# Performance work log

Measured on AMD Instinct MI355X. Metric: run time of the kernel, lower is better.

The kernel has to match this reference:

```python
import jax, jax.numpy as jnp
import numpy as np

L, B, E, H = 2048, 2, 1024, 16
HD = E // H


def setup_inputs() -> dict:
    key = jax.random.key(0)
    ks = jax.random.split(key, 7)
    return {
        "query": jax.random.normal(ks[0], (L, B, E), dtype=jnp.float32),
        "key": jax.random.normal(ks[1], (L, B, E), dtype=jnp.float32),
        "value": jax.random.normal(ks[2], (L, B, E), dtype=jnp.float32),
        "in_proj_weight": jax.random.normal(ks[3], (3 * E, E), dtype=jnp.float32) * 0.02,
        "in_proj_bias": jax.random.normal(ks[4], (3 * E,), dtype=jnp.float32) * 0.02,
        "out_proj_weight": jax.random.normal(ks[5], (E, E), dtype=jnp.float32) * 0.02,
        "out_proj_bias": jax.random.normal(ks[6], (E,), dtype=jnp.float32) * 0.02,
    }


def reference(query, key, value, in_proj_weight, in_proj_bias, out_proj_weight, out_proj_bias):
    l, b, e = query.shape
    scaling = jnp.asarray(HD, query.dtype) ** -0.5
    wq, wk, wv = jnp.split(in_proj_weight, 3, axis=0)
    bq, bk, bv = jnp.split(in_proj_bias, 3)
    q = (query @ wq.T + bq) * scaling          # [L,B,E]
    k = key @ wk.T + bk
    v = value @ wv.T + bv

    def to_heads(t):  # [L,B,E] -> [B*H, L, HD]
        return t.reshape(l, b * H, HD).transpose(1, 0, 2)

    q, k, v = to_heads(q), to_heads(k), to_heads(v)
    scores = jnp.einsum('nld,nmd->nlm', q, k)  # [B*H, L, L] materialized as in legacy MHA
    attn = jax.nn.softmax(scores, axis=-1)
    out = jnp.einsum('nlm,nmd->nld', attn, v)  # [B*H, L, HD]
    out = out.transpose(1, 0, 2).reshape(l, b, e)
    return out @ out_proj_weight.T + out_proj_bias
```

## Files before the change

### kernel.cpp

```cpp
#include <hip/hip_runtime.h>
#include <hip/hip_bf16.h>

typedef __attribute__((ext_vector_type(8))) short short8;
typedef __attribute__((ext_vector_type(4))) float floatx4;
typedef __attribute__((ext_vector_type(16))) float floatx16;

#define L_SEQ 2048
#define EMB   1024
#define HD    64
#define QSCALE 0.18033688011112042f
#define FIXMAX2 11.541560327111707f

__device__ __forceinline__ unsigned short f2bf(float f) {
    unsigned int u = __float_as_uint(f);
    u += 0x7fffu + ((u >> 16) & 1u);
    return (unsigned short)(u >> 16);
}
__device__ __forceinline__ unsigned pkbf(float a, float b) {
    return (unsigned)f2bf(a) | ((unsigned)f2bf(b) << 16);
}
__device__ __forceinline__ unsigned pkbf2(float a, float b) {
    __hip_bfloat162 h = __float22bfloat162_rn(make_float2(a, b));
    unsigned u; __builtin_memcpy(&u, &h, 4); return u;
}
__device__ __forceinline__ void gld_lds16(const void* g, void* l) {
    __builtin_amdgcn_global_load_lds(
        (const __attribute__((address_space(1))) unsigned*)g,
        (__attribute__((address_space(3))) unsigned*)l, 16, 0, 0);
}
__device__ __forceinline__ float fexp2(float x) {
    return __builtin_amdgcn_exp2f(x);
}

__global__ __launch_bounds__(256) void convert_all(
    const float* __restrict__ q, const float* __restrict__ k,
    const float* __restrict__ v, const float* __restrict__ ipw,
    const float* __restrict__ opw,
    unsigned short* __restrict__ Abq, unsigned short* __restrict__ Abk,
    unsigned short* __restrict__ Abv, unsigned short* __restrict__ Wipb,
    unsigned short* __restrict__ Wopb)
{
    const int NA = 1048576, NIP = 786432;
    int idx = blockIdx.x * 256 + threadIdx.x;
    const float* src; unsigned short* dst; int o;
    if (idx < NA)            { src = q;   dst = Abq;  o = idx; }
    else if (idx < 2 * NA)   { src = k;   dst = Abk;  o = idx - NA; }
    else if (idx < 3 * NA)   { src = v;   dst = Abv;  o = idx - 2 * NA; }
    else if (idx < 3 * NA + NIP) { src = ipw; dst = Wipb; o = idx - 3 * NA; }
    else                     { src = opw; dst = Wopb; o = idx - 3 * NA - NIP; }
    float4 f = ((const float4*)src)[o];
    ((uint2*)dst)[o] = make_uint2(pkbf(f.x, f.y), pkbf(f.z, f.w));
}

__global__ __launch_bounds__(256, 3) void qkv_gemm(
    const unsigned short* __restrict__ Abq, const unsigned short* __restrict__ Abk,
    const unsigned short* __restrict__ Abv, const unsigned short* __restrict__ Wb,
    const float* __restrict__ Bip,
    unsigned short* __restrict__ Qh, unsigned short* __restrict__ Kf,
    unsigned short* __restrict__ Vf)
{
    __shared__ unsigned short lds[17408];
    unsigned short* As = lds;
    unsigned short* Bs = lds + 8192;

    const int tid = threadIdx.x, lane = tid & 63, w = tid >> 6;
    const int wm = (w & 1) * 64, wn = (w >> 1) * 64;
    const int m0 = blockIdx.x * 128, n0 = blockIdx.y * 128;
    const int cn = lane & 15, g = lane >> 4;
    const int z = n0 >> 10;
    const unsigned short* Ag = (z == 0) ? Abq : (z == 1) ? Abk : Abv;

    floatx4 acc[4][4];
    #pragma unroll
    for (int i = 0; i < 4; ++i)
        #pragma unroll
        for (int j = 0; j < 4; ++j) acc[i][j] = (floatx4){0.f, 0.f, 0.f, 0.f};

    for (int k0 = 0; k0 < EMB; k0 += 64) {
        __syncthreads();
        #pragma unroll
        for (int p = 0; p < 4; ++p) {
            int u0 = (p * 4 + w) * 64, u = u0 + lane, row = u >> 3, sl = u & 7;
            gld_lds16(Ag + (size_t)(m0 + row) * EMB + k0 + ((sl ^ (row & 7)) * 8), &As[u0 * 8]);
            gld_lds16(Wb + (size_t)(n0 + row) * EMB + k0 + ((sl ^ (row & 7)) * 8), &Bs[u0 * 8]);
        }
        __syncthreads();
        #pragma unroll
        for (int kc = 0; kc < 2; ++kc) {
            short8 a4[4], b4[4];
            #pragma unroll
            for (int i = 0; i < 4; ++i)
                a4[i] = *(const short8*)&As[(wm + i * 16 + cn) * 64 + (((kc * 4 + g) ^ (cn & 7)) * 8)];
            #pragma unroll
            for (int j = 0; j < 4; ++j)
                b4[j] = *(const short8*)&Bs[(wn + j * 16 + cn) * 64 + (((kc * 4 + g) ^ (cn & 7)) * 8)];
            #pragma unroll
            for (int i = 0; i < 4; ++i)
                #pragma unroll
                for (int j = 0; j < 4; ++j)
                    acc[i][j] = __builtin_amdgcn_mfma_f32_16x16x32_bf16(a4[i], b4[j], acc[i][j], 0, 0, 0);
        }
    }

    if (z == 0) {
        #pragma unroll
        for (int j = 0; j < 4; ++j) {
            int col = n0 + wn + j * 16 + cn;
            float bv = Bip[col];
            int o = col & 1023, h = o >> 6, d = o & 63;
            #pragma unroll
            for (int i = 0; i < 4; ++i)
                #pragma unroll
                for (int r = 0; r < 4; ++r) {
                    int rr = m0 + wm + i * 16 + g * 4 + r;
                    float vv = acc[i][j][r] + bv;
                    int l = rr >> 1, bb = rr & 1, nn = bb * 16 + h;
                    Qh[((size_t)nn * L_SEQ + l) * HD + d] = f2bf(vv * QSCALE);
                }
        }
    } else if (z == 1) {
        __syncthreads();
        #pragma unroll
        for (int j = 0; j < 4; ++j) {
            int cl = wn + j * 16 + cn;
            float bv = Bip[n0 + cl];
            #pragma unroll
            for (int i = 0; i < 4; ++i)
                #pragma unroll
                for (int r = 0; r < 4; ++r) {
                    int rr = wm + i * 16 + g * 4 + r;
                    lds[rr * 136 + cl] = f2bf(acc[i][j][r] + bv);
                }
        }
        __syncthreads();
        const int h0 = (n0 - 1024) >> 6;
        const int b = w >> 1, hl = w & 1;
        const int nn = b * 16 + h0 + hl;
        const int c32l = lane & 31, hi5 = lane >> 5;
        #pragma unroll
        for (int cc = 0; cc < 8; ++cc) {
            int t32l = cc >> 2, kk = cc & 3;
            int rr = (t32l * 32 + c32l) * 2 + b;
            int ccol = hl * 64 + kk * 16 + hi5 * 8;
            uint4 val = *(const uint4*)&lds[rr * 136 + ccol];
            int ck = (nn * 64 + (m0 >> 6) + t32l) * 4 + kk;
            *(uint4*)(Kf + (size_t)ck * 512 + lane * 8) = val;
        }
    } else {
        __syncthreads();
        #pragma unroll
        for (int j = 0; j < 4; ++j) {
            int col_l = wn + j * 16 + cn;
            float bv = Bip[n0 + col_l];
            #pragma unroll
            for (int i = 0; i < 4; ++i) {
                int rrb = wm + i * 16 + g * 4;
                int l0 = rrb >> 1;
                float v0 = acc[i][j][0] + bv, v1 = acc[i][j][1] + bv;
                float v2 = acc[i][j][2] + bv, v3 = acc[i][j][3] + bv;
                *(unsigned*)&lds[col_l * 136 +      l0] = pkbf(v0, v2);
                *(unsigned*)&lds[col_l * 136 + 64 + l0] = pkbf(v1, v3);
            }
        }
        __syncthreads();
        const int h0 = (n0 - 2048) >> 6;
        const int b = w >> 1, hl = w & 1;
        const int nn = b * 16 + h0 + hl;
        const int c32l = lane & 31, hi5 = lane >> 5;
        #pragma unroll
        for (int cc = 0; cc < 8; ++cc) {
            int dt = cc >> 2, kk2l = cc & 3;
            int col_l = hl * 64 + dt * 32 + c32l;
            int keyl = kk2l * 16 + hi5 * 8;
            uint4 val = *(const uint4*)&lds[col_l * 136 + b * 64 + keyl];
            int cv = nn * 256 + ((m0 >> 5) + kk2l) * 2 + dt;
            *(uint4*)(Vf + (size_t)cv * 512 + lane * 8) = val;
        }
    }
}

__global__ __launch_bounds__(256, 2) void flash_attn_k(
    const unsigned short* __restrict__ Qh, const unsigned short* __restrict__ Kf,
    const unsigned short* __restrict__ Vf, unsigned short* __restrict__ Oh)
{
    const int id = blockIdx.y * 32 + blockIdx.x;
    const int xcd = id & 7, slot = id >> 3;
    const int n = xcd * 4 + (slot & 3);
    const int q0 = (slot >> 2) * 64;

    __shared__ float Uf[2 * 64 * 67];

    const int tid = threadIdx.x, lane = tid & 63, w = tid >> 6;
    const int c32 = lane & 31, hi = lane >> 5;

    short8 qf[2][4];
    #pragma unroll
    for (int qt = 0; qt < 2; ++qt)
        #pragma unroll
        for (int kk = 0; kk < 4; ++kk)
            qf[qt][kk] = *(const short8*)(Qh + ((size_t)n * L_SEQ + q0 + qt * 32 + c32) * HD + kk * 16 + hi * 8);

    floatx16 acc_o[2][2];
    #pragma unroll
    for (int qt = 0; qt < 2; ++qt)
        #pragma unroll
        for (int dt = 0; dt < 2; ++dt)
            #pragma unroll
            for (int r = 0; r < 16; ++r) acc_o[qt][dt][r] = 0.f;
    float lsum0 = 0.f, lsum1 = 0.f;

    const unsigned short* kp = Kf + ((size_t)n * 256 + w * 64) * 512 + lane * 8;
    const unsigned short* vp = Vf + ((size_t)n * 256 + w * 64) * 512 + lane * 8;

    for (int t = 0; t < 16; ++t) {
        short8 kf[4], vf[2][2];
        #pragma unroll
        for (int kk = 0; kk < 4; ++kk)
            kf[kk] = *(const short8*)(kp + kk * 512);
        #pragma unroll
        for (int kc = 0; kc < 2; ++kc)
            #pragma unroll
            for (int dt = 0; dt < 2; ++dt)
                vf[kc][dt] = *(const short8*)(vp + (kc * 2 + dt) * 512);
        kp += 2048; vp += 2048;

        floatx16 s[2];
        #pragma unroll
        for (int qt = 0; qt < 2; ++qt) {
            #pragma unroll
            for (int r = 0; r < 16; ++r) s[qt][r] = -FIXMAX2;
            __builtin_amdgcn_s_setprio(1);
            #pragma unroll
            for (int kk = 0; kk < 4; ++kk)
                s[qt] = __builtin_amdgcn_mfma_f32_32x32x16_bf16(kf[kk], qf[qt][kk], s[qt], 0, 0, 0);
            __builtin_amdgcn_s_setprio(0);
        }

        #pragma unroll
        for (int qt = 0; qt < 2; ++qt) {
            float p[16];
            #pragma unroll
            for (int r = 0; r < 16; ++r) p[r] = fexp2(s[qt][r]);
            float ls = ((p[0] + p[1]) + (p[2] + p[3])) + ((p[4] + p[5]) + (p[6] + p[7]))
                     + ((p[8] + p[9]) + (p[10] + p[11])) + ((p[12] + p[13]) + (p[14] + p[15]));
            if (qt == 0) lsum0 += ls; else lsum1 += ls;

            short8 pa[2];
            #pragma unroll
            for (int kc = 0; kc < 2; ++kc) {
                unsigned A = pkbf2(p[kc * 8 + 0], p[kc * 8 + 1]);
                unsigned B = pkbf2(p[kc * 8 + 2], p[kc * 8 + 3]);
                unsigned C = pkbf2(p[kc * 8 + 4], p[kc * 8 + 5]);
                unsigned D = pkbf2(p[kc * 8 + 6], p[kc * 8 + 7]);
                asm("v_permlane32_swap_b32 %0, %1" : "+v"(A), "+v"(C));
                asm("v_permlane32_swap_b32 %0, %1" : "+v"(B), "+v"(D));
                union { unsigned u[4]; short8 v; } cv;
                cv.u[0] = A; cv.u[1] = B; cv.u[2] = C; cv.u[3] = D;
                pa[kc] = cv.v;
            }

            __builtin_amdgcn_s_setprio(1);
            #pragma unroll
            for (int kc = 0; kc < 2; ++kc)
                #pragma unroll
                for (int dt = 0; dt < 2; ++dt)
                    acc_o[qt][dt] = __builtin_amdgcn_mfma_f32_32x32x16_bf16(pa[kc], vf[kc][dt], acc_o[qt][dt], 0, 0, 0);
            __builtin_amdgcn_s_setprio(0);
        }
    }

    {
        float a0 = lsum0, b0 = lsum0;
        asm("v_permlane32_swap_b32 %0, %1" : "+v"(a0), "+v"(b0));
        lsum0 = a0 + b0;
        float a1 = lsum1, b1 = lsum1;
        asm("v_permlane32_swap_b32 %0, %1" : "+v"(a1), "+v"(b1));
        lsum1 = a1 + b1;
    }

#define BLOB_STORE(base) do {                                              \
    _Pragma("unroll")                                                      \
    for (int qt = 0; qt < 2; ++qt)                                         \
        _Pragma("unroll")                                                  \
        for (int dt = 0; dt < 2; ++dt)                                     \
            _Pragma("unroll")                                              \
            for (int r = 0; r < 16; ++r)                                   \
                Uf[(base) + (qt * 2 + dt) * 16 + r] = acc_o[qt][dt][r];    \
    Uf[(base) + 64] = lsum0; Uf[(base) + 65] = lsum1;                      \
} while (0)
#define BLOB_ADD(base) do {                                                \
    _Pragma("unroll")                                                      \
    for (int qt = 0; qt < 2; ++qt)                                         \
        _Pragma("unroll")                                                  \
        for (int dt = 0; dt < 2; ++dt)                                     \
            _Pragma("unroll")                                              \
            for (int r = 0; r < 16; ++r)                                   \
                acc_o[qt][dt][r] += Uf[(base) + (qt * 2 + dt) * 16 + r];   \
    lsum0 += Uf[(base) + 64]; lsum1 += Uf[(base) + 65];                    \
} while (0)

    const int r0 = lane * 67, r1 = 64 * 67 + lane * 67;
    __syncthreads();
    if (w == 1) BLOB_STORE(r0);
    if (w == 3) BLOB_STORE(r1);
    __syncthreads();
    if (w == 0) BLOB_ADD(r0);
    if (w == 2) { BLOB_ADD(r1); BLOB_STORE(r1); }
    __syncthreads();
    if (w == 0) {
        BLOB_ADD(r1);
        float inv0 = 1.0f / lsum0, inv1 = 1.0f / lsum1;
        const int hib = hi * 16;
        const int bb = n >> 4, h = n & 15;
        #pragma unroll
        for (int qt = 0; qt < 2; ++qt) {
            float invq = qt ? inv1 : inv0;
            #pragma unroll
            for (int r = 0; r < 16; ++r) {
                int idx = ((r & 3) + 8 * (r >> 2)) * 4 + hib;
                float invr = __int_as_float(__builtin_amdgcn_ds_bpermute(idx, __float_as_int(invq)));
                int q = q0 + qt * 32 + (r & 3) + 8 * (r >> 2) + hi * 4;
                #pragma unroll
                for (int dt = 0; dt < 2; ++dt) {
                    int e = h * 64 + dt * 32 + c32;
                    Oh[((size_t)q * 2 + bb) * EMB + e] = f2bf(acc_o[qt][dt][r] * invr);
                }
            }
        }
    }
#undef BLOB_STORE
#undef BLOB_ADD
}

__global__ __launch_bounds__(256, 3) void out_gemm(
    const unsigned short* __restrict__ Oh, const unsigned short* __restrict__ Wob,
    const float* __restrict__ bo, float* __restrict__ out)
{
    __shared__ unsigned short As[128 * 64];
    __shared__ unsigned short Bs[128 * 64];

    const int tid = threadIdx.x, lane = tid & 63, w = tid >> 6;
    const int wm = (w & 1) * 64, wn = (w >> 1) * 64;
    const int m0 = blockIdx.x * 128, n0 = blockIdx.y * 128;
    const int cn = lane & 15, g = lane >> 4;

    floatx4 acc[4][4];
    #pragma unroll
    for (int i = 0; i < 4; ++i)
        #pragma unroll
        for (int j = 0; j < 4; ++j) acc[i][j] = (floatx4){0.f, 0.f, 0.f, 0.f};

    for (int k0 = 0; k0 < EMB; k0 += 64) {
        __syncthreads();
        #pragma unroll
        for (int p = 0; p < 4; ++p) {
            int u0 = (p * 4 + w) * 64, u = u0 + lane, row = u >> 3, sl = u & 7;
            gld_lds16(Oh  + (size_t)(m0 + row) * EMB + k0 + ((sl ^ (row & 7)) * 8), &As[u0 * 8]);
            gld_lds16(Wob + (size_t)(n0 + row) * EMB + k0 + ((sl ^ (row & 7)) * 8), &Bs[u0 * 8]);
        }
        __syncthreads();
        #pragma unroll
        for (int kc = 0; kc < 2; ++kc) {
            short8 a4[4], b4[4];
            #pragma unroll
            for (int i = 0; i < 4; ++i)
                a4[i] = *(const short8*)&As[(wm + i * 16 + cn) * 64 + (((kc * 4 + g) ^ (cn & 7)) * 8)];
            #pragma unroll
            for (int j = 0; j < 4; ++j)
                b4[j] = *(const short8*)&Bs[(wn + j * 16 + cn) * 64 + (((kc * 4 + g) ^ (cn & 7)) * 8)];
            #pragma unroll
            for (int i = 0; i < 4; ++i)
                #pragma unroll
                for (int j = 0; j < 4; ++j)
                    acc[i][j] = __builtin_amdgcn_mfma_f32_16x16x32_bf16(a4[i], b4[j], acc[i][j], 0, 0, 0);
        }
    }

    #pragma unroll
    for (int j = 0; j < 4; ++j) {
        int col = n0 + wn + j * 16 + cn;
        float bv = bo[col];
        #pragma unroll
        for (int i = 0; i < 4; ++i)
            #pragma unroll
            for (int r = 0; r < 4; ++r)
                out[(size_t)(m0 + wm + i * 16 + g * 4 + r) * EMB + col] = acc[i][j][r] + bv;
    }
}

extern "C" void kernel_launch(void* const* d_in, const int* in_sizes, int n_in,
                              void* d_out, int out_size, void* d_ws, size_t ws_size,
                              hipStream_t stream) {
    const float* q   = (const float*)d_in[0];
    const float* k   = (const float*)d_in[1];
    const float* v   = (const float*)d_in[2];
    const float* ipw = (const float*)d_in[3];
    const float* ipb = (const float*)d_in[4];
    const float* opw = (const float*)d_in[5];
    const float* opb = (const float*)d_in[6];
    float* out = (float*)d_out;

    const size_t HE = (size_t)32 * L_SEQ * HD;
    unsigned short* Qh   = (unsigned short*)d_ws;
    unsigned short* Kf   = Qh + HE;
    unsigned short* Vf   = Kf + HE;
    unsigned short* Wipb = Vf + HE;
    unsigned short* Wopb = Wipb + (size_t)3 * EMB * EMB;
    unsigned short* Abq  = Wopb + (size_t)EMB * EMB;
    unsigned short* Abk  = Abq + HE;
    unsigned short* Abv  = Abk + HE;
    unsigned short* Oh   = Abq;

    convert_all<<<dim3(16384), 256, 0, stream>>>(q, k, v, ipw, opw, Abq, Abk, Abv, Wipb, Wopb);
    qkv_gemm<<<dim3(32, 24), 256, 0, stream>>>(Abq, Abk, Abv, Wipb, ipb, Qh, Kf, Vf);
    flash_attn_k<<<dim3(32, 32), 256, 0, stream>>>(Qh, Kf, Vf, Oh);
    out_gemm<<<dim3(32, 8), 256, 0, stream>>>(Oh, Wopb, opb, out);
}
```

Baseline: 210.7 us.

## Stage Q epilogue through LDS into fragment layout; halve out_gemm M tile

```diff
diff --git a/kernel.cpp b/kernel.cpp
--- a/kernel.cpp
+++ b/kernel.cpp
@@ -56,7 +56,7 @@
     const unsigned short* __restrict__ Abq, const unsigned short* __restrict__ Abk,
     const unsigned short* __restrict__ Abv, const unsigned short* __restrict__ Wb,
     const float* __restrict__ Bip,
-    unsigned short* __restrict__ Qh, unsigned short* __restrict__ Kf,
+    unsigned short* __restrict__ Qf, unsigned short* __restrict__ Kf,
     unsigned short* __restrict__ Vf)
 {
     __shared__ unsigned short lds[17408];
@@ -102,23 +102,10 @@
         }
     }
 
-    if (z == 0) {
-        #pragma unroll
-        for (int j = 0; j < 4; ++j) {
-            int col = n0 + wn + j * 16 + cn;
-            float bv = Bip[col];
-            int o = col & 1023, h = o >> 6, d = o & 63;
-            #pragma unroll
-            for (int i = 0; i < 4; ++i)
-                #pragma unroll
-                for (int r = 0; r < 4; ++r) {
-                    int rr = m0 + wm + i * 16 + g * 4 + r;
-                    float vv = acc[i][j][r] + bv;
-                    int l = rr >> 1, bb = rr & 1, nn = bb * 16 + h;
-                    Qh[((size_t)nn * L_SEQ + l) * HD + d] = f2bf(vv * QSCALE);
-                }
-        }
-    } else if (z == 1) {
+    const int c32l = lane & 31, hi5 = lane >> 5;
+    const int b = w >> 1, hl = w & 1;
+
+    if (z < 2) {
         __syncthreads();
         #pragma unroll
         for (int j = 0; j < 4; ++j) {
@@ -129,14 +116,14 @@
                 #pragma unroll
                 for (int r = 0; r < 4; ++r) {
                     int rr = wm + i * 16 + g * 4 + r;
-                    lds[rr * 136 + cl] = f2bf(acc[i][j][r] + bv);
+                    float vv = acc[i][j][r] + bv;
+                    lds[rr * 136 + cl] = f2bf(z == 0 ? vv * QSCALE : vv);
                 }
         }
         __syncthreads();
-        const int h0 = (n0 - 1024) >> 6;
-        const int b = w >> 1, hl = w & 1;
+        const int h0 = (n0 & 1023) >> 6;
         const int nn = b * 16 + h0 + hl;
-        const int c32l = lane & 31, hi5 = lane >> 5;
+        unsigned short* Dst = (z == 0) ? Qf : Kf;
         #pragma unroll
         for (int cc = 0; cc < 8; ++cc) {
             int t32l = cc >> 2, kk = cc & 3;
@@ -144,7 +131,7 @@
             int ccol = hl * 64 + kk * 16 + hi5 * 8;
             uint4 val = *(const uint4*)&lds[rr * 136 + ccol];
             int ck = (nn * 64 + (m0 >> 6) + t32l) * 4 + kk;
-            *(uint4*)(Kf + (size_t)ck * 512 + lane * 8) = val;
+            *(uint4*)(Dst + (size_t)ck * 512 + lane * 8) = val;
         }
     } else {
         __syncthreads();
@@ -164,9 +151,7 @@
         }
         __syncthreads();
         const int h0 = (n0 - 2048) >> 6;
-        const int b = w >> 1, hl = w & 1;
         const int nn = b * 16 + h0 + hl;
-        const int c32l = lane & 31, hi5 = lane >> 5;
         #pragma unroll
         for (int cc = 0; cc < 8; ++cc) {
             int dt = cc >> 2, kk2l = cc & 3;
@@ -180,7 +165,7 @@
 }
 
 __global__ __launch_bounds__(256, 2) void flash_attn_k(
-    const unsigned short* __restrict__ Qh, const unsigned short* __restrict__ Kf,
+    const unsigned short* __restrict__ Qf, const unsigned short* __restrict__ Kf,
     const unsigned short* __restrict__ Vf, unsigned short* __restrict__ Oh)
 {
     const int id = blockIdx.y * 32 + blockIdx.x;
@@ -198,7 +183,7 @@
     for (int qt = 0; qt < 2; ++qt)
         #pragma unroll
         for (int kk = 0; kk < 4; ++kk)
-            qf[qt][kk] = *(const short8*)(Qh + ((size_t)n * L_SEQ + q0 + qt * 32 + c32) * HD + kk * 16 + hi * 8);
+            qf[qt][kk] = *(const short8*)(Qf + ((size_t)((n * 64 + (q0 >> 5) + qt) * 4 + kk)) * 512 + lane * 8);
 
     floatx16 acc_o[2][2];
     #pragma unroll
@@ -332,21 +317,21 @@
 #undef BLOB_ADD
 }
 
-__global__ __launch_bounds__(256, 3) void out_gemm(
+__global__ __launch_bounds__(256, 4) void out_gemm(
     const unsigned short* __restrict__ Oh, const unsigned short* __restrict__ Wob,
     const float* __restrict__ bo, float* __restrict__ out)
 {
-    __shared__ unsigned short As[128 * 64];
+    __shared__ unsigned short As[64 * 64];
     __shared__ unsigned short Bs[128 * 64];
 
     const int tid = threadIdx.x, lane = tid & 63, w = tid >> 6;
-    const int wm = (w & 1) * 64, wn = (w >> 1) * 64;
-    const int m0 = blockIdx.x * 128, n0 = blockIdx.y * 128;
+    const int wm = (w & 1) * 32, wn = (w >> 1) * 64;
+    const int m0 = blockIdx.x * 64, n0 = blockIdx.y * 128;
     const int cn = lane & 15, g = lane >> 4;
 
-    floatx4 acc[4][4];
+    floatx4 acc[2][4];
     #pragma unroll
-    for (int i = 0; i < 4; ++i)
+    for (int i = 0; i < 2; ++i)
         #pragma unroll
         for (int j = 0; j < 4; ++j) acc[i][j] = (floatx4){0.f, 0.f, 0.f, 0.f};
 
@@ -355,21 +340,22 @@
         #pragma unroll
         for (int p = 0; p < 4; ++p) {
             int u0 = (p * 4 + w) * 64, u = u0 + lane, row = u >> 3, sl = u & 7;
-            gld_lds16(Oh  + (size_t)(m0 + row) * EMB + k0 + ((sl ^ (row & 7)) * 8), &As[u0 * 8]);
+            if (p < 2)
+                gld_lds16(Oh + (size_t)(m0 + row) * EMB + k0 + ((sl ^ (row & 7)) * 8), &As[u0 * 8]);
             gld_lds16(Wob + (size_t)(n0 + row) * EMB + k0 + ((sl ^ (row & 7)) * 8), &Bs[u0 * 8]);
         }
         __syncthreads();
         #pragma unroll
         for (int kc = 0; kc < 2; ++kc) {
-            short8 a4[4], b4[4];
-            #pragma unroll
-            for (int i = 0; i < 4; ++i)
+            short8 a4[2], b4[4];
+            #pragma unroll
+            for (int i = 0; i < 2; ++i)
                 a4[i] = *(const short8*)&As[(wm + i * 16 + cn) * 64 + (((kc * 4 + g) ^ (cn & 7)) * 8)];
             #pragma unroll
             for (int j = 0; j < 4; ++j)
                 b4[j] = *(const short8*)&Bs[(wn + j * 16 + cn) * 64 + (((kc * 4 + g) ^ (cn & 7)) * 8)];
             #pragma unroll
-            for (int i = 0; i < 4; ++i)
+            for (int i = 0; i < 2; ++i)
                 #pragma unroll
                 for (int j = 0; j < 4; ++j)
                     acc[i][j] = __builtin_amdgcn_mfma_f32_16x16x32_bf16(a4[i], b4[j], acc[i][j], 0, 0, 0);
@@ -381,7 +367,7 @@
         int col = n0 + wn + j * 16 + cn;
         float bv = bo[col];
         #pragma unroll
-        for (int i = 0; i < 4; ++i)
+        for (int i = 0; i < 2; ++i)
             #pragma unroll
             for (int r = 0; r < 4; ++r)
                 out[(size_t)(m0 + wm + i * 16 + g * 4 + r) * EMB + col] = acc[i][j][r] + bv;
@@ -401,8 +387,8 @@
     float* out = (float*)d_out;
 
     const size_t HE = (size_t)32 * L_SEQ * HD;
-    unsigned short* Qh   = (unsigned short*)d_ws;
-    unsigned short* Kf   = Qh + HE;
+    unsigned short* Qf   = (unsigned short*)d_ws;
+    unsigned short* Kf   = Qf + HE;
     unsigned short* Vf   = Kf + HE;
     unsigned short* Wipb = Vf + HE;
     unsigned short* Wopb = Wipb + (size_t)3 * EMB * EMB;
@@ -412,7 +398,7 @@
     unsigned short* Oh   = Abq;
 
     convert_all<<<dim3(16384), 256, 0, stream>>>(q, k, v, ipw, opw, Abq, Abk, Abv, Wipb, Wopb);
-    qkv_gemm<<<dim3(32, 24), 256, 0, stream>>>(Abq, Abk, Abv, Wipb, ipb, Qh, Kf, Vf);
-    flash_attn_k<<<dim3(32, 32), 256, 0, stream>>>(Qh, Kf, Vf, Oh);
-    out_gemm<<<dim3(32, 8), 256, 0, stream>>>(Oh, Wopb, opb, out);
-}
+    qkv_gemm<<<dim3(32, 24), 256, 0, stream>>>(Abq, Abk, Abv, Wipb, ipb, Qf, Kf, Vf);
+    flash_attn_k<<<dim3(32, 32), 256, 0, stream>>>(Qf, Kf, Vf, Oh);
+    out_gemm<<<dim3(64, 8), 256, 0, stream>>>(Oh, Wopb, opb, out);
+}
```

Result: no change. 207.2 us (-1.7%).
